# Kernel optimization log

Hardware: AMD Instinct MI355X
Metric: run time of the kernel (lower is better)

Reference implementation:

```python
import jax, jax.numpy as jnp
import numpy as np

N_NODES = 16384
H = 128


def setup_inputs() -> dict:
    key = jax.random.key(0)
    k1, k2, k3, k4, k5 = jax.random.split(key, 5)
    neighbour_h = jax.random.normal(k1, (N_NODES, 2, H), dtype=jnp.float32)
    A = jax.random.uniform(k2, (H, H, 3 * H), dtype=jnp.float32)  # th.rand
    U1_w = jax.random.normal(k3, (3 * H, H), dtype=jnp.float32)   # Linear weight (out,in), no bias
    U2_w = jax.random.normal(k4, (3 * H, H), dtype=jnp.float32)
    U2_b = jax.random.normal(k5, (3 * H,), dtype=jnp.float32)
    return {"neighbour_h": neighbour_h, "A": A, "U1_w": U1_w, "U2_w": U2_w, "U2_b": U2_b}


def reference(neighbour_h, A, U1_w, U2_w, U2_b):
    # compute_iou_gate of BinaryFullTensorCell (pos_stationarity=False)
    n, _, h = neighbour_h.shape
    h1 = neighbour_h[:, 0, :]  # (n, h)
    h2 = neighbour_h[:, 1, :]  # (n, h)
    # bilinear: einsum('ijk,ni,nj->nk') -- contract via per-node outer product
    # then a single GEMM against A reshaped to (h*h, 3h).
    outer = h1[:, :, None] * h2[:, None, :]          # (n, h, h)
    bil = outer.reshape(n, h * h) @ A.reshape(h * h, -1)  # (n, 3h)
    # torch Linear: x @ W.T (+ b)
    out = bil + h1 @ U1_w.T + h2 @ U2_w.T + U2_b
    return out
```

## Files before the change

### kernel.cpp

```cpp
#include <hip/hip_runtime.h>
#include <hip/hip_bf16.h>

typedef __attribute__((ext_vector_type(8))) short bf16x8;
typedef __attribute__((ext_vector_type(16))) float f32x16;
typedef __attribute__((ext_vector_type(4))) float f32x4;
typedef __attribute__((ext_vector_type(4))) unsigned int uint4v;
typedef unsigned short ushort_t;
typedef unsigned int uint_t;

#define N_NODES 16384
#define HD 128
#define NOUT 384
#define PART_ELEMS 6291456

static __device__ __forceinline__ ushort_t f2bf(float f) {
  __hip_bfloat16 b = __float2bfloat16(f);
  return *reinterpret_cast<ushort_t*>(&b);
}

__global__ void prep_all(const float* __restrict__ A, const float* __restrict__ U1,
                         const float* __restrict__ U2, const float* __restrict__ nh,
                         ushort_t* __restrict__ pk, ushort_t* __restrict__ h1,
                         ushort_t* __restrict__ h2, float* __restrict__ h1tf) {
  __shared__ __align__(16) char smem[49152];
  const int b = blockIdx.x;
  const int t = threadIdx.x;

  if (b < 260) {
    short* spk = reinterpret_cast<short*>(smem);
    const int half = b & 1;
    const int gg = t >> 5, ll = t & 31;
    if (b < 256) {
      const int it = b >> 1;
      const size_t krow0 = (size_t)it * 128 + half * 64;
#pragma unroll 4
      for (int kl = 0; kl < 64; ++kl) {
        float v = A[(krow0 + kl) * NOUT + t];
        int cl = kl >> 4, oc = (kl >> 3) & 1, j = kl & 7;
        spk[(gg * 8 + cl * 2 + oc) * 256 + ll * 8 + j] = f2bf(v);
      }
    } else {
      const int u = (b - 256) >> 1;
      const float* U = u ? U2 : U1;
#pragma unroll 4
      for (int kl = 0; kl < 64; ++kl) {
        float v = U[(size_t)t * HD + half * 64 + kl];
        int cl = kl >> 4, oc = (kl >> 3) & 1, j = kl & 7;
        spk[(gg * 8 + cl * 2 + oc) * 256 + ll * 8 + j] = f2bf(v);
      }
    }
    __syncthreads();
    const int it_out = (b < 256) ? (b >> 1) : (128 + ((b - 256) >> 1));
    const int f = t * 64;
    const int g = f >> 11;
    const int inner = f & 2047;
    ushort_t* dst = pk + (size_t)it_out * 49152 + g * 4096 + half * 2048 + inner;
    const uint4* src = reinterpret_cast<const uint4*>(spk + f);
    uint4* d4 = reinterpret_cast<uint4*>(dst);
#pragma unroll
    for (int q = 0; q < 8; ++q) d4[q] = src[q];
  } else {
    if (t < 256) {
      float (*sm)[65] = reinterpret_cast<float(*)[65]>(smem);
      const int g = b - 260;
      const int mt = g & 255, jt = g >> 8;
      const int tx = t & 63, ty = t >> 6;
      const int m0 = mt * 64, j0 = jt * 64;
#pragma unroll
      for (int s = 0; s < 16; ++s) {
        int mm = ty + s * 4;
        float f1 = nh[(size_t)(m0 + mm) * 256 + j0 + tx];
        float f2 = nh[(size_t)(m0 + mm) * 256 + 128 + j0 + tx];
        h1[(size_t)(m0 + mm) * HD + j0 + tx] = f2bf(f1);
        h2[(size_t)(m0 + mm) * HD + j0 + tx] = f2bf(f2);
        sm[mm][tx] = f1;
      }
      __syncthreads();
#pragma unroll
      for (int s = 0; s < 16; ++s) {
        int jj = ty + s * 4;
        h1tf[(size_t)(j0 + jj) * N_NODES + m0 + tx] = sm[tx][jj];
      }
    }
  }
}

#define PK_STEP 98304
#define SLICE_B 16896

#define STAGE(IT, R)                                                              \
  do {                                                                            \
    const char* s_ = pkbase + (size_t)(IT) * PK_STEP + stg;                       \
    char* d_ = ldsb + (R) * SLICE_B + wv * 4096;                                  \
    __builtin_amdgcn_global_load_lds((const uint_t*)(s_),        (uint_t*)(d_),        16, 0, 0); \
    __builtin_amdgcn_global_load_lds((const uint_t*)(s_ + 1024), (uint_t*)(d_ + 1024), 16, 0, 0); \
    __builtin_amdgcn_global_load_lds((const uint_t*)(s_ + 2048), (uint_t*)(d_ + 2048), 16, 0, 0); \
    __builtin_amdgcn_global_load_lds((const uint_t*)(s_ + 3072), (uint_t*)(d_ + 3072), 16, 0, 0); \
    const int ith_ = (IT) < 128 ? (IT) : 127;                                     \
    const char* h_ = reinterpret_cast<const char*>(                               \
                         h1tf + (size_t)ith_ * N_NODES + Mt * 128) + wv * 128;    \
    if (lane < 8)                                                                 \
      __builtin_amdgcn_global_load_lds((const uint_t*)(h_ + lane * 16),           \
          (uint_t*)(ldsb + (R) * SLICE_B + 16384 + wv * 128), 16, 0, 0);          \
  } while (0)

#define READN(BBN, SN0, SN1, RN)                                                  \
  do {                                                                            \
    const char* lb_ = ldsb + (RN) * SLICE_B;                                      \
    const char* bb_ = lb_ + wn * 8192 + oct * 512 + l31 * 16;                     \
    SN0 = *reinterpret_cast<const float*>(lb_ + 16384 + (wm * 64 + l31) * 4);     \
    SN1 = *reinterpret_cast<const float*>(lb_ + 16384 + (wm * 64 + 32 + l31) * 4);\
    _Pragma("unroll")                                                             \
    for (int c = 0; c < 8; ++c)                                                   \
      BBN[c] = *reinterpret_cast<const uint4v*>(bb_ + c * 1024);                  \
  } while (0)

#define CHAINRD(BBC, PC0, PC1, BBN, SN0, SN1, RN)                                 \
  do {                                                                            \
    const char* lb_ = ldsb + (RN) * SLICE_B;                                      \
    const char* bb_ = lb_ + wn * 8192 + oct * 512 + l31 * 16;                     \
    SN0 = *reinterpret_cast<const float*>(lb_ + 16384 + (wm * 64 + l31) * 4);     \
    SN1 = *reinterpret_cast<const float*>(lb_ + 16384 + (wm * 64 + 32 + l31) * 4);\
    PC0 = vz; PC1 = vz;                                                           \
    _Pragma("unroll")                                                             \
    for (int c = 0; c < 8; ++c) {                                                 \
      BBN[c] = *reinterpret_cast<const uint4v*>(bb_ + c * 1024);                  \
      bf16x8 f_ = __builtin_bit_cast(bf16x8, BBC[c]);                             \
      PC0 = __builtin_amdgcn_mfma_f32_32x32x16_bf16(                              \
          f_, __builtin_bit_cast(bf16x8, h2u[0][c]), PC0, 0, 0, 0);               \
      PC1 = __builtin_amdgcn_mfma_f32_32x32x16_bf16(                              \
          f_, __builtin_bit_cast(bf16x8, h2u[1][c]), PC1, 0, 0, 0);               \
    }                                                                             \
  } while (0)

#define CHAIN(BBC, PC0, PC1)                                                      \
  do {                                                                            \
    PC0 = vz; PC1 = vz;                                                           \
    _Pragma("unroll")                                                             \
    for (int c = 0; c < 8; ++c) {                                                 \
      bf16x8 f_ = __builtin_bit_cast(bf16x8, BBC[c]);                             \
      PC0 = __builtin_amdgcn_mfma_f32_32x32x16_bf16(                              \
          f_, __builtin_bit_cast(bf16x8, h2u[0][c]), PC0, 0, 0, 0);               \
      PC1 = __builtin_amdgcn_mfma_f32_32x32x16_bf16(                              \
          f_, __builtin_bit_cast(bf16x8, h2u[1][c]), PC1, 0, 0, 0);               \
    }                                                                             \
  } while (0)

#define TAIL(S0_, S1_, PP0, PP1)                                                  \
  do {                                                                            \
    _Pragma("unroll")                                                             \
    for (int rr = 0; rr < 16; ++rr) {                                             \
      acc[0][rr] += (S0_) * PP0[rr];                                              \
      acc[1][rr] += (S1_) * PP1[rr];                                              \
    }                                                                             \
  } while (0)

__global__ __launch_bounds__(256, 2)
void gemm_kernel(const ushort_t* __restrict__ pk, const ushort_t* __restrict__ h1bf,
                 const ushort_t* __restrict__ h2bf, const float* __restrict__ h1tf,
                 const float* __restrict__ u2b, float* __restrict__ part) {
  __shared__ __align__(16) char ldsb[3 * SLICE_B];

  const int tid = threadIdx.x;
  const int bid = blockIdx.x;
  const int v  = (bid & 7) * 192 + (bid >> 3);
  const int Mt = v & 127;
  const int q  = v >> 7;
  const int Nt = q >> 1;
  const int ks = q & 1;

  const int lane = tid & 63, wv = tid >> 6;
  const int l31 = lane & 31, oct = lane >> 5;
  const int wm = wv >> 1, wn = wv & 1;
  const int mbase = Mt * 128 + wm * 64;
  const int n0w = Nt * 64 + wn * 32;
  const int g0 = Nt * 2;

  uint4v h2u[2][8];
#pragma unroll
  for (int ms = 0; ms < 2; ++ms) {
    const ushort_t* hp = h2bf + (size_t)(mbase + ms * 32 + l31) * HD + oct * 8;
#pragma unroll
    for (int c = 0; c < 8; ++c)
      h2u[ms][c] = *reinterpret_cast<const uint4v*>(hp + c * 16);
  }

  f32x16 acc[2];
  if (ks) {
#pragma unroll
    for (int qq = 0; qq < 4; ++qq) {
      f32x4 bq = *reinterpret_cast<const f32x4*>(u2b + n0w + 8 * qq + 4 * oct);
#pragma unroll
      for (int j = 0; j < 4; ++j) { acc[0][qq * 4 + j] = bq[j]; acc[1][qq * 4 + j] = bq[j]; }
    }
  } else {
    acc[0] = (f32x16)(0.0f);
    acc[1] = (f32x16)(0.0f);
  }

  const int it0 = ks ? 65 : 0;
  const int it1 = ks ? 128 : 65;

  const char* pkbase = reinterpret_cast<const char*>(pk) + (size_t)g0 * 8192;
  const int stg = wv * 4096 + lane * 16;

  const f32x16 vz = (f32x16)(0.0f);

  STAGE(it0, 0);
  STAGE(it0 + 1, 1);
  asm volatile("s_waitcnt vmcnt(5)" ::: "memory");
  __builtin_amdgcn_s_barrier();
  uint4v bbX[8], bbY[8];
  f32x16 pX0, pX1, pY0 = vz, pY1 = vz;
  float sX0, sX1, sY0 = 0.0f, sY1 = 0.0f;
  READN(bbX, sX0, sX1, 0);

  int rn = 1, rsb = 2;
  for (int it = it0; it + 1 < it1; it += 2) {
    {
      const float t0 = sY0, t1 = sY1;
      STAGE(it + 2, rsb); rsb = (rsb == 2) ? 0 : rsb + 1;
      asm volatile("s_waitcnt vmcnt(5)" ::: "memory");
      __builtin_amdgcn_s_barrier();
      CHAINRD(bbX, pX0, pX1, bbY, sY0, sY1, rn); rn = (rn == 2) ? 0 : rn + 1;
      TAIL(t0, t1, pY0, pY1);
    }
    {
      const float t0 = sX0, t1 = sX1;
      STAGE(it + 3, rsb); rsb = (rsb == 2) ? 0 : rsb + 1;
      asm volatile("s_waitcnt vmcnt(5)" ::: "memory");
      __builtin_amdgcn_s_barrier();
      CHAINRD(bbY, pY0, pY1, bbX, sX0, sX1, rn); rn = (rn == 2) ? 0 : rn + 1;
      TAIL(t0, t1, pX0, pX1);
    }
  }
  {
    TAIL(sY0, sY1, pY0, pY1);
    CHAIN(bbX, pX0, pX1);
    TAIL(sX0, sX1, pX0, pX1);
  }

  if (ks) {
    const char* bt = reinterpret_cast<const char*>(pk) +
                     (size_t)128 * PK_STEP + (size_t)((g0 + wn) * 16 + oct) * 512 +
                     (size_t)l31 * 16;
#pragma unroll
    for (int c = 0; c < 8; ++c) {
      bf16x8 bfr = __builtin_bit_cast(bf16x8, *reinterpret_cast<const uint4v*>(bt + c * 1024));
#pragma unroll
      for (int ms = 0; ms < 2; ++ms) {
        bf16x8 a = *reinterpret_cast<const bf16x8*>(
            h1bf + (size_t)(mbase + ms * 32 + l31) * HD + c * 16 + oct * 8);
        acc[ms] = __builtin_amdgcn_mfma_f32_32x32x16_bf16(bfr, a, acc[ms], 0, 0, 0);
      }
    }
    const char* bt2 = bt + PK_STEP;
#pragma unroll
    for (int c = 0; c < 8; ++c) {
      bf16x8 bfr = __builtin_bit_cast(bf16x8, *reinterpret_cast<const uint4v*>(bt2 + c * 1024));
#pragma unroll
      for (int ms = 0; ms < 2; ++ms) {
        acc[ms] = __builtin_amdgcn_mfma_f32_32x32x16_bf16(
            bfr, __builtin_bit_cast(bf16x8, h2u[ms][c]), acc[ms], 0, 0, 0);
      }
    }
  }

  float* my = part + (size_t)ks * PART_ELEMS;
#pragma unroll
  for (int ms = 0; ms < 2; ++ms) {
    float* rowp = my + (size_t)(mbase + ms * 32 + l31) * NOUT + n0w + 4 * oct;
#pragma unroll
    for (int qq = 0; qq < 4; ++qq) {
      f32x4 o;
      o[0] = acc[ms][qq * 4 + 0];
      o[1] = acc[ms][qq * 4 + 1];
      o[2] = acc[ms][qq * 4 + 2];
      o[3] = acc[ms][qq * 4 + 3];
      *reinterpret_cast<f32x4*>(rowp + 8 * qq) = o;
    }
  }
}

__global__ void reduce2(const float* __restrict__ part, float* __restrict__ out) {
  int i = blockIdx.x * 256 + threadIdx.x;
  float4 a = reinterpret_cast<const float4*>(part)[i];
  float4 b = reinterpret_cast<const float4*>(part + PART_ELEMS)[i];
  float4 o;
  o.x = a.x + b.x; o.y = a.y + b.y; o.z = a.z + b.z; o.w = a.w + b.w;
  reinterpret_cast<float4*>(out)[i] = o;
}

extern "C" void kernel_launch(void* const* d_in, const int* in_sizes, int n_in,
                              void* d_out, int out_size, void* d_ws, size_t ws_size,
                              hipStream_t stream) {
  const float* nh  = (const float*)d_in[0];
  const float* A   = (const float*)d_in[1];
  const float* U1  = (const float*)d_in[2];
  const float* U2  = (const float*)d_in[3];
  const float* U2b = (const float*)d_in[4];

  char* ws = (char*)d_ws;
  ushort_t* pk   = (ushort_t*)(ws);
  ushort_t* h1bf = (ushort_t*)(ws + 12779520);
  ushort_t* h2bf = (ushort_t*)(ws + 16973824);
  float*    h1tf = (float*)(ws + 21168128);
  float*    part = (float*)(ws + 29556736);

  prep_all<<<dim3(772), 384, 0, stream>>>(A, U1, U2, nh, pk, h1bf, h2bf, h1tf);
  gemm_kernel<<<dim3(1536), 256, 0, stream>>>(pk, h1bf, h2bf, h1tf, U2b, part);
  reduce2<<<dim3(6144), 256, 0, stream>>>(part, (float*)d_out);
}
```

Baseline: 292.4 us.

## Fuse split-K reduction into GEMM via atomic tile counters and add MFMA setprio

Removes the separate reduce2 kernel. The two split-K blocks for each output tile now pick roles with an atomic counter: the first writes its partial to the workspace and raises a flag, and the second spins on that flag, then adds the partial and writes the final output. This halves partial-buffer traffic and drops one kernel launch, at the cost of a memset, a spin-wait, and a potential deadlock if the second block is resident while the first is not scheduled. It also raises wave priority around the MFMA chains with s_setprio.

```diff
diff --git a/kernel.cpp b/kernel.cpp
--- a/kernel.cpp
+++ b/kernel.cpp
@@ -11,7 +11,6 @@
 #define N_NODES 16384
 #define HD 128
 #define NOUT 384
-#define PART_ELEMS 6291456
 
 static __device__ __forceinline__ ushort_t f2bf(float f) {
   __hip_bfloat16 b = __float2bfloat16(f);
@@ -122,6 +121,7 @@
     SN0 = *reinterpret_cast<const float*>(lb_ + 16384 + (wm * 64 + l31) * 4);     \
     SN1 = *reinterpret_cast<const float*>(lb_ + 16384 + (wm * 64 + 32 + l31) * 4);\
     PC0 = vz; PC1 = vz;                                                           \
+    __builtin_amdgcn_s_setprio(1);                                                \
     _Pragma("unroll")                                                             \
     for (int c = 0; c < 8; ++c) {                                                 \
       BBN[c] = *reinterpret_cast<const uint4v*>(bb_ + c * 1024);                  \
@@ -131,11 +131,13 @@
       PC1 = __builtin_amdgcn_mfma_f32_32x32x16_bf16(                              \
           f_, __builtin_bit_cast(bf16x8, h2u[1][c]), PC1, 0, 0, 0);               \
     }                                                                             \
+    __builtin_amdgcn_s_setprio(0);                                                \
   } while (0)
 
 #define CHAIN(BBC, PC0, PC1)                                                      \
   do {                                                                            \
     PC0 = vz; PC1 = vz;                                                           \
+    __builtin_amdgcn_s_setprio(1);                                                \
     _Pragma("unroll")                                                             \
     for (int c = 0; c < 8; ++c) {                                                 \
       bf16x8 f_ = __builtin_bit_cast(bf16x8, BBC[c]);                             \
@@ -144,6 +146,7 @@
       PC1 = __builtin_amdgcn_mfma_f32_32x32x16_bf16(                              \
           f_, __builtin_bit_cast(bf16x8, h2u[1][c]), PC1, 0, 0, 0);               \
     }                                                                             \
+    __builtin_amdgcn_s_setprio(0);                                                \
   } while (0)
 
 #define TAIL(S0_, S1_, PP0, PP1)                                                  \
@@ -158,8 +161,10 @@
 __global__ __launch_bounds__(256, 2)
 void gemm_kernel(const ushort_t* __restrict__ pk, const ushort_t* __restrict__ h1bf,
                  const ushort_t* __restrict__ h2bf, const float* __restrict__ h1tf,
-                 const float* __restrict__ u2b, float* __restrict__ part) {
+                 const float* __restrict__ u2b, float* __restrict__ part,
+                 float* __restrict__ out, uint_t* __restrict__ ctrl) {
   __shared__ __align__(16) char ldsb[3 * SLICE_B];
+  __shared__ int role_sh;
 
   const int tid = threadIdx.x;
   const int bid = blockIdx.x;
@@ -266,29 +271,55 @@
     }
   }
 
-  float* my = part + (size_t)ks * PART_ELEMS;
-#pragma unroll
-  for (int ms = 0; ms < 2; ++ms) {
-    float* rowp = my + (size_t)(mbase + ms * 32 + l31) * NOUT + n0w + 4 * oct;
-#pragma unroll
-    for (int qq = 0; qq < 4; ++qq) {
-      f32x4 o;
-      o[0] = acc[ms][qq * 4 + 0];
-      o[1] = acc[ms][qq * 4 + 1];
-      o[2] = acc[ms][qq * 4 + 2];
-      o[3] = acc[ms][qq * 4 + 3];
-      *reinterpret_cast<f32x4*>(rowp + 8 * qq) = o;
-    }
-  }
-}
-
-__global__ void reduce2(const float* __restrict__ part, float* __restrict__ out) {
-  int i = blockIdx.x * 256 + threadIdx.x;
-  float4 a = reinterpret_cast<const float4*>(part)[i];
-  float4 b = reinterpret_cast<const float4*>(part + PART_ELEMS)[i];
-  float4 o;
-  o.x = a.x + b.x; o.y = a.y + b.y; o.z = a.z + b.z; o.w = a.w + b.w;
-  reinterpret_cast<float4*>(out)[i] = o;
+  const int tile = Mt * 6 + Nt;
+  uint_t* cnt = ctrl + tile * 2;
+  uint_t* flg = cnt + 1;
+  if (tid == 0)
+    role_sh = (int)__hip_atomic_fetch_add(cnt, 1u, __ATOMIC_RELAXED,
+                                          __HIP_MEMORY_SCOPE_AGENT);
+  __syncthreads();
+
+  if (role_sh == 0) {
+#pragma unroll
+    for (int ms = 0; ms < 2; ++ms) {
+      float* rowp = part + (size_t)(mbase + ms * 32 + l31) * NOUT + n0w + 4 * oct;
+#pragma unroll
+      for (int qq = 0; qq < 4; ++qq) {
+        f32x4 o;
+        o[0] = acc[ms][qq * 4 + 0];
+        o[1] = acc[ms][qq * 4 + 1];
+        o[2] = acc[ms][qq * 4 + 2];
+        o[3] = acc[ms][qq * 4 + 3];
+        *reinterpret_cast<f32x4*>(rowp + 8 * qq) = o;
+      }
+    }
+    __threadfence();
+    __syncthreads();
+    if (tid == 0)
+      __hip_atomic_store(flg, 1u, __ATOMIC_RELEASE, __HIP_MEMORY_SCOPE_AGENT);
+  } else {
+    if (tid == 0) {
+      while (__hip_atomic_load(flg, __ATOMIC_ACQUIRE, __HIP_MEMORY_SCOPE_AGENT) == 0)
+        __builtin_amdgcn_s_sleep(8);
+    }
+    __syncthreads();
+    __threadfence();
+#pragma unroll
+    for (int ms = 0; ms < 2; ++ms) {
+      const float* prow = part + (size_t)(mbase + ms * 32 + l31) * NOUT + n0w + 4 * oct;
+      float* orow = out + (size_t)(mbase + ms * 32 + l31) * NOUT + n0w + 4 * oct;
+#pragma unroll
+      for (int qq = 0; qq < 4; ++qq) {
+        f32x4 p = *reinterpret_cast<const f32x4*>(prow + 8 * qq);
+        f32x4 o;
+        o[0] = acc[ms][qq * 4 + 0] + p[0];
+        o[1] = acc[ms][qq * 4 + 1] + p[1];
+        o[2] = acc[ms][qq * 4 + 2] + p[2];
+        o[3] = acc[ms][qq * 4 + 3] + p[3];
+        *reinterpret_cast<f32x4*>(orow + 8 * qq) = o;
+      }
+    }
+  }
 }
 
 extern "C" void kernel_launch(void* const* d_in, const int* in_sizes, int n_in,
@@ -306,8 +337,10 @@
   ushort_t* h2bf = (ushort_t*)(ws + 16973824);
   float*    h1tf = (float*)(ws + 21168128);
   float*    part = (float*)(ws + 29556736);
-
+  uint_t*   ctrl = (uint_t*)(ws + 54722560);
+
+  hipMemsetAsync(ctrl, 0, 768 * 2 * sizeof(uint_t), stream);
   prep_all<<<dim3(772), 384, 0, stream>>>(A, U1, U2, nh, pk, h1bf, h2bf, h1tf);
-  gemm_kernel<<<dim3(1536), 256, 0, stream>>>(pk, h1bf, h2bf, h1tf, U2b, part);
-  reduce2<<<dim3(6144), 256, 0, stream>>>(part, (float*)d_out);
+  gemm_kernel<<<dim3(1536), 256, 0, stream>>>(pk, h1bf, h2bf, h1tf, U2b, part,
+                                              (float*)d_out, ctrl);
 }
```

Result: slower. 523.4 us (+79.0%).

## Remove split-K partials and reduce kernel; each block computes full K range

Applied to the files above, without the earlier changes.

The two-way split-K is dropped, so each block now loops over all 128 K slices and writes the final output directly. This removes the partial-sum buffer traffic and the separate reduce launch. The U1 and U2 slices are folded into the pipeline tail through the staged LDS buffers, and launch bounds are raised to 3 blocks per CU to make up for the grid being halved to 768 blocks. The trade-off is less parallelism, longer per-block serial work, and tighter register pressure.

```diff
diff --git a/kernel.cpp b/kernel.cpp
--- a/kernel.cpp
+++ b/kernel.cpp
@@ -11,7 +11,6 @@
 #define N_NODES 16384
 #define HD 128
 #define NOUT 384
-#define PART_ELEMS 6291456
 
 static __device__ __forceinline__ ushort_t f2bf(float f) {
   __hip_bfloat16 b = __float2bfloat16(f);
@@ -133,19 +132,6 @@
     }                                                                             \
   } while (0)
 
-#define CHAIN(BBC, PC0, PC1)                                                      \
-  do {                                                                            \
-    PC0 = vz; PC1 = vz;                                                           \
-    _Pragma("unroll")                                                             \
-    for (int c = 0; c < 8; ++c) {                                                 \
-      bf16x8 f_ = __builtin_bit_cast(bf16x8, BBC[c]);                             \
-      PC0 = __builtin_amdgcn_mfma_f32_32x32x16_bf16(                              \
-          f_, __builtin_bit_cast(bf16x8, h2u[0][c]), PC0, 0, 0, 0);               \
-      PC1 = __builtin_amdgcn_mfma_f32_32x32x16_bf16(                              \
-          f_, __builtin_bit_cast(bf16x8, h2u[1][c]), PC1, 0, 0, 0);               \
-    }                                                                             \
-  } while (0)
-
 #define TAIL(S0_, S1_, PP0, PP1)                                                  \
   do {                                                                            \
     _Pragma("unroll")                                                             \
@@ -155,19 +141,17 @@
     }                                                                             \
   } while (0)
 
-__global__ __launch_bounds__(256, 2)
+__global__ __launch_bounds__(256, 3)
 void gemm_kernel(const ushort_t* __restrict__ pk, const ushort_t* __restrict__ h1bf,
                  const ushort_t* __restrict__ h2bf, const float* __restrict__ h1tf,
-                 const float* __restrict__ u2b, float* __restrict__ part) {
+                 const float* __restrict__ u2b, float* __restrict__ out) {
   __shared__ __align__(16) char ldsb[3 * SLICE_B];
 
   const int tid = threadIdx.x;
   const int bid = blockIdx.x;
-  const int v  = (bid & 7) * 192 + (bid >> 3);
+  const int v  = (bid & 7) * 96 + (bid >> 3);
   const int Mt = v & 127;
-  const int q  = v >> 7;
-  const int Nt = q >> 1;
-  const int ks = q & 1;
+  const int Nt = v >> 7;
 
   const int lane = tid & 63, wv = tid >> 6;
   const int l31 = lane & 31, oct = lane >> 5;
@@ -186,28 +170,20 @@
   }
 
   f32x16 acc[2];
-  if (ks) {
-#pragma unroll
-    for (int qq = 0; qq < 4; ++qq) {
-      f32x4 bq = *reinterpret_cast<const f32x4*>(u2b + n0w + 8 * qq + 4 * oct);
-#pragma unroll
-      for (int j = 0; j < 4; ++j) { acc[0][qq * 4 + j] = bq[j]; acc[1][qq * 4 + j] = bq[j]; }
-    }
-  } else {
-    acc[0] = (f32x16)(0.0f);
-    acc[1] = (f32x16)(0.0f);
-  }
-
-  const int it0 = ks ? 65 : 0;
-  const int it1 = ks ? 128 : 65;
+#pragma unroll
+  for (int qq = 0; qq < 4; ++qq) {
+    f32x4 bq = *reinterpret_cast<const f32x4*>(u2b + n0w + 8 * qq + 4 * oct);
+#pragma unroll
+    for (int j = 0; j < 4; ++j) { acc[0][qq * 4 + j] = bq[j]; acc[1][qq * 4 + j] = bq[j]; }
+  }
 
   const char* pkbase = reinterpret_cast<const char*>(pk) + (size_t)g0 * 8192;
   const int stg = wv * 4096 + lane * 16;
 
   const f32x16 vz = (f32x16)(0.0f);
 
-  STAGE(it0, 0);
-  STAGE(it0 + 1, 1);
+  STAGE(0, 0);
+  STAGE(1, 1);
   asm volatile("s_waitcnt vmcnt(5)" ::: "memory");
   __builtin_amdgcn_s_barrier();
   uint4v bbX[8], bbY[8];
@@ -216,7 +192,7 @@
   READN(bbX, sX0, sX1, 0);
 
   int rn = 1, rsb = 2;
-  for (int it = it0; it + 1 < it1; it += 2) {
+  for (int it = 0; it + 1 < 128; it += 2) {
     {
       const float t0 = sY0, t1 = sY1;
       STAGE(it + 2, rsb); rsb = (rsb == 2) ? 0 : rsb + 1;
@@ -234,30 +210,27 @@
       TAIL(t0, t1, pX0, pX1);
     }
   }
+  TAIL(sY0, sY1, pY0, pY1);
+
+#pragma unroll
+  for (int c = 0; c < 8; ++c) {
+    bf16x8 bfr = __builtin_bit_cast(bf16x8, bbX[c]);
+#pragma unroll
+    for (int ms = 0; ms < 2; ++ms) {
+      bf16x8 a = *reinterpret_cast<const bf16x8*>(
+          h1bf + (size_t)(mbase + ms * 32 + l31) * HD + c * 16 + oct * 8);
+      acc[ms] = __builtin_amdgcn_mfma_f32_32x32x16_bf16(bfr, a, acc[ms], 0, 0, 0);
+    }
+  }
+
+  asm volatile("s_waitcnt vmcnt(0)" ::: "memory");
+  __builtin_amdgcn_s_barrier();
   {
-    TAIL(sY0, sY1, pY0, pY1);
-    CHAIN(bbX, pX0, pX1);
-    TAIL(sX0, sX1, pX0, pX1);
-  }
-
-  if (ks) {
-    const char* bt = reinterpret_cast<const char*>(pk) +
-                     (size_t)128 * PK_STEP + (size_t)((g0 + wn) * 16 + oct) * 512 +
-                     (size_t)l31 * 16;
+    float du0, du1;
+    READN(bbY, du0, du1, rn);
 #pragma unroll
     for (int c = 0; c < 8; ++c) {
-      bf16x8 bfr = __builtin_bit_cast(bf16x8, *reinterpret_cast<const uint4v*>(bt + c * 1024));
-#pragma unroll
-      for (int ms = 0; ms < 2; ++ms) {
-        bf16x8 a = *reinterpret_cast<const bf16x8*>(
-            h1bf + (size_t)(mbase + ms * 32 + l31) * HD + c * 16 + oct * 8);
-        acc[ms] = __builtin_amdgcn_mfma_f32_32x32x16_bf16(bfr, a, acc[ms], 0, 0, 0);
-      }
-    }
-    const char* bt2 = bt + PK_STEP;
-#pragma unroll
-    for (int c = 0; c < 8; ++c) {
-      bf16x8 bfr = __builtin_bit_cast(bf16x8, *reinterpret_cast<const uint4v*>(bt2 + c * 1024));
+      bf16x8 bfr = __builtin_bit_cast(bf16x8, bbY[c]);
 #pragma unroll
       for (int ms = 0; ms < 2; ++ms) {
         acc[ms] = __builtin_amdgcn_mfma_f32_32x32x16_bf16(
@@ -266,10 +239,9 @@
     }
   }
 
-  float* my = part + (size_t)ks * PART_ELEMS;
 #pragma unroll
   for (int ms = 0; ms < 2; ++ms) {
-    float* rowp = my + (size_t)(mbase + ms * 32 + l31) * NOUT + n0w + 4 * oct;
+    float* rowp = out + (size_t)(mbase + ms * 32 + l31) * NOUT + n0w + 4 * oct;
 #pragma unroll
     for (int qq = 0; qq < 4; ++qq) {
       f32x4 o;
@@ -280,15 +252,6 @@
       *reinterpret_cast<f32x4*>(rowp + 8 * qq) = o;
     }
   }
-}
-
-__global__ void reduce2(const float* __restrict__ part, float* __restrict__ out) {
-  int i = blockIdx.x * 256 + threadIdx.x;
-  float4 a = reinterpret_cast<const float4*>(part)[i];
-  float4 b = reinterpret_cast<const float4*>(part + PART_ELEMS)[i];
-  float4 o;
-  o.x = a.x + b.x; o.y = a.y + b.y; o.z = a.z + b.z; o.w = a.w + b.w;
-  reinterpret_cast<float4*>(out)[i] = o;
 }
 
 extern "C" void kernel_launch(void* const* d_in, const int* in_sizes, int n_in,
@@ -305,9 +268,7 @@
   ushort_t* h1bf = (ushort_t*)(ws + 12779520);
   ushort_t* h2bf = (ushort_t*)(ws + 16973824);
   float*    h1tf = (float*)(ws + 21168128);
-  float*    part = (float*)(ws + 29556736);
 
   prep_all<<<dim3(772), 384, 0, stream>>>(A, U1, U2, nh, pk, h1bf, h2bf, h1tf);
-  gemm_kernel<<<dim3(1536), 256, 0, stream>>>(pk, h1bf, h2bf, h1tf, U2b, part);
-  reduce2<<<dim3(6144), 256, 0, stream>>>(part, (float*)d_out);
-}
+  gemm_kernel<<<dim3(768), 256, 0, stream>>>(pk, h1bf, h2bf, h1tf, U2b, (float*)d_out);
+}
```

Measured after the change: 743.5 us. 154% more time.
